# Kernel optimization log

Hardware: AMD Instinct MI355X
Metric: run time of the kernel (lower is better)

## Reference

```python
import jax, jax.numpy as jnp
import numpy as np

N_E = 1024
E_DIM = 64
BETA = 0.25


def setup_inputs() -> dict:
    key = jax.random.key(0)
    k_z, k_c = jax.random.split(key)
    z = jax.random.normal(k_z, (64, E_DIM, 32, 32), dtype=jnp.float32)  # [B, e_dim, H, W]
    # Codebook initialized uniform(-1/n_e, 1/n_e) as in the torch module
    codebook = jax.random.uniform(k_c, (N_E, E_DIM), dtype=jnp.float32,
                                  minval=-1.0 / N_E, maxval=1.0 / N_E)
    return {"z": z, "codebook": codebook}


def reference(z, codebook):
    beta = BETA
    n_e, e_dim = codebook.shape
    # [B, e_dim, H, W] -> [B, H, W, e_dim]
    z_nhwc = jnp.transpose(z, (0, 2, 3, 1))
    zf = z_nhwc.reshape(-1, e_dim)  # [N, e_dim]
    # Squared Euclidean distances: ||z||^2 + ||e||^2 - 2 z.e  -> [N, n_e]
    d = (jnp.sum(zf * zf, axis=1, keepdims=True)
         + jnp.sum(codebook * codebook, axis=1)
         - 2.0 * jnp.matmul(zf, codebook.T))
    min_encoding_indices = jnp.argmin(d, axis=1)[:, None]  # [N, 1]
    min_encodings = jax.nn.one_hot(min_encoding_indices[:, 0], n_e, dtype=zf.dtype)  # [N, n_e]
    # Gather codebook rows via one-hot matmul (same math as torch version)
    z_q = jnp.matmul(min_encodings, codebook).reshape(z_nhwc.shape)  # [B,H,W,e_dim]
    sg = jax.lax.stop_gradient
    loss = (jnp.mean((sg(z_nhwc) - z_q) ** 2)
            + beta * jnp.mean((z_nhwc - sg(z_q)) ** 2))
    # Straight-through estimator
    z_q = z_nhwc + sg(z_q - z_nhwc)
    z_q = jnp.transpose(z_q, (0, 3, 1, 2))  # back to [B, e_dim, H, W]
    return (loss, z_q, min_encodings, min_encoding_indices)
```

## Files before the change

kernel.cpp:

```cpp
#include <hip/hip_runtime.h>

#define N_ROWS 65536
#define NE 1024
#define ED 64
#define ERR_GAP 8e-5f

static const size_t OFF_ZQ = 1;
static const size_t OFF_ME = 1 + 4194304;
static const size_t OFF_IDX = OFF_ME + (size_t)N_ROWS * NE;
#define ME_FLOATS ((size_t)N_ROWS * NE)

#define SC_CBF  0
#define SC_Z2   65536
#define SC_FLAG 131072
#define SC_CAND 196608

typedef __attribute__((ext_vector_type(8))) short short8v;
typedef __attribute__((ext_vector_type(4))) float f32x4;

__device__ __forceinline__ unsigned bf16_rne(float v) {
  unsigned u = __float_as_uint(v);
  return (u + 0x7FFFu + ((u >> 16) & 1u)) >> 16;
}

__device__ __forceinline__ void gld16(const void* g, void* l) {
  __builtin_amdgcn_global_load_lds(
      (const __attribute__((address_space(1))) void*)g,
      (__attribute__((address_space(3))) void*)l, 16, 0, 0);
}

__global__ __launch_bounds__(256) void k_fill(float* __restrict__ me) {
  const size_t n4 = (ME_FLOATS - 3) >> 2;
  float4* __restrict__ p4 = reinterpret_cast<float4*>(me + 3);
  const size_t stride = (size_t)gridDim.x * blockDim.x;
  const float4 zero4 = make_float4(0.f, 0.f, 0.f, 0.f);
  for (size_t i = blockIdx.x * (size_t)blockDim.x + threadIdx.x; i < n4; i += stride)
    p4[i] = zero4;
  if (blockIdx.x == 0 && threadIdx.x == 0) {
    me[0] = 0.f; me[1] = 0.f; me[2] = 0.f;
    me[ME_FLOATS - 1] = 0.f;
  }
}

__global__ __launch_bounds__(256) void k_e2cb(const float* __restrict__ cb,
                                              float* __restrict__ e2,
                                              short* __restrict__ cbfrag) {
  const int tid = blockIdx.x * 256 + threadIdx.x;
  const int ct = tid >> 6, lane = tid & 63;
  const int col = ct * 16 + (lane & 15);
  const int k0 = (lane >> 4) * 8;
  const float* __restrict__ ep = cb + (size_t)col * ED + k0;
  short* __restrict__ o = cbfrag + (size_t)ct * 2048 + lane * 8;
  #pragma unroll
  for (int ks = 0; ks < 2; ++ks) {
    short h[8], lo[8];
    #pragma unroll
    for (int i = 0; i < 8; ++i) {
      const float v = ep[ks * 32 + i];
      const unsigned hb = bf16_rne(v);
      const float res = v - __uint_as_float(hb << 16);
      h[i] = (short)hb; lo[i] = (short)bf16_rne(res);
    }
    *(short8v*)(o + (size_t)(0 * 2 + ks) * 512) = *(short8v*)h;
    *(short8v*)(o + (size_t)(1 * 2 + ks) * 512) = *(short8v*)lo;
  }
  if (threadIdx.x < 64) {
    const int j = blockIdx.x * 64 + threadIdx.x;
    const float* __restrict__ e = cb + (size_t)j * ED;
    float r[8];
    #pragma unroll
    for (int i = 0; i < 8; ++i) {
      float v = e[i]; float q = v * v;
      asm volatile("" : "+v"(q)); r[i] = q;
    }
    #pragma unroll
    for (int k = 1; k < 8; ++k)
      #pragma unroll
      for (int i = 0; i < 8; ++i) {
        float v = e[8 * k + i]; float q = v * v;
        asm volatile("" : "+v"(q)); r[i] += q;
      }
    e2[j] = ((r[0] + r[1]) + (r[2] + r[3])) + ((r[4] + r[5]) + (r[6] + r[7]));
  }
}

__global__ __launch_bounds__(256, 4) void k_dist(const float* __restrict__ z,
    const short* __restrict__ cbfrag, const float* __restrict__ e2g,
    float* __restrict__ z2g, float* __restrict__ idxf, int* __restrict__ flag,
    int* __restrict__ cand) {
  __shared__ float4 smem4[2320];
  short* lBs = (short*)smem4;
  float* e2l = (float*)(smem4 + 2048);
  float* z2l = (float*)(smem4 + 2304);
  float (*lzf)[65] = (float(*)[65])smem4;

  const int t = threadIdx.x, w = t >> 6, lane = t & 63;
  const int row0 = blockIdx.x * 64;

  gld16(e2g + w * 256 + lane * 4, e2l + w * 256);

  const int rl = w * 16 + (lane & 15);
  const int n0 = row0 + rl;
  const int bb = n0 >> 10, hw = n0 & 1023;
  const float* __restrict__ zp = z + (size_t)bb * 65536 + hw;
  const int k0 = (lane >> 4) * 8;
  #pragma unroll
  for (int ks = 0; ks < 2; ++ks)
    #pragma unroll
    for (int i = 0; i < 8; ++i)
      lzf[ks * 32 + k0 + i][rl] = zp[(size_t)(ks * 32 + k0 + i) << 10];
  __syncthreads();

  short8v a[2][2];
  #pragma unroll
  for (int ks = 0; ks < 2; ++ks) {
    short h[8], lo[8];
    #pragma unroll
    for (int i = 0; i < 8; ++i) {
      const float v = lzf[ks * 32 + k0 + i][rl];
      const unsigned hb = bf16_rne(v);
      const float res = v - __uint_as_float(hb << 16);
      h[i] = (short)hb; lo[i] = (short)bf16_rne(res);
    }
    a[0][ks] = *(short8v*)h;
    a[1][ks] = *(short8v*)lo;
  }
  if (t < 64) {
    float r[8];
    #pragma unroll
    for (int i = 0; i < 8; ++i) {
      const float v = lzf[i][t];
      float q = v * v; asm volatile("" : "+v"(q)); r[i] = q;
    }
    #pragma unroll
    for (int k = 1; k < 8; ++k)
      #pragma unroll
      for (int i = 0; i < 8; ++i) {
        const float v = lzf[8 * k + i][t];
        float q = v * v; asm volatile("" : "+v"(q)); r[i] += q;
      }
    const float z2v = ((r[0] + r[1]) + (r[2] + r[3])) + ((r[4] + r[5]) + (r[6] + r[7]));
    z2g[row0 + t] = z2v;
    z2l[t] = z2v;
  }
  __syncthreads();

  #pragma unroll
  for (int i = 0; i < 4; ++i) {
    const int s = w * 4 + i;
    gld16(cbfrag + s * 512 + lane * 8, lBs + s * 512);
  }
  float z2r[4];
  #pragma unroll
  for (int reg = 0; reg < 4; ++reg)
    z2r[reg] = z2l[w * 16 + (lane >> 4) * 4 + reg];
  float Tm1[4], Tm2[4], Tm3[4]; int Tb1[4], Tb2[4];
  #pragma unroll
  for (int reg = 0; reg < 4; ++reg) {
    Tm1[reg] = 1e30f; Tm2[reg] = 1e30f; Tm3[reg] = 1e30f;
    Tb1[reg] = 0; Tb2[reg] = 0;
  }
  __syncthreads();

  int buf = 0;
  for (int c = 0; c < 16; ++c) {
    if (c < 15) {
      #pragma unroll
      for (int i = 0; i < 4; ++i) {
        const int s = w * 4 + i;
        gld16(cbfrag + (size_t)(c + 1) * 8192 + s * 512 + lane * 8,
              lBs + (buf ^ 1) * 8192 + s * 512);
      }
    }
    #pragma unroll 1
    for (int ctl = 0; ctl < 4; ++ctl) {
      short8v bfr[2][2];
      #pragma unroll
      for (int hl = 0; hl < 2; ++hl)
        #pragma unroll
        for (int ks = 0; ks < 2; ++ks)
          bfr[hl][ks] = *(const short8v*)(lBs + buf * 8192 +
              (ctl * 4 + hl * 2 + ks) * 512 + lane * 8);

      f32x4 acc = (f32x4)(0.0f);
      #pragma unroll
      for (int p = 0; p < 3; ++p) {
        const int pa = (p == 2) ? 1 : 0;
        const int pb = (p == 1) ? 1 : 0;
        #pragma unroll
        for (int ks = 0; ks < 2; ++ks)
          acc = __builtin_amdgcn_mfma_f32_16x16x32_bf16(a[pa][ks], bfr[pb][ks], acc, 0, 0, 0);
      }
      const int j = c * 64 + ctl * 16 + (lane & 15);
      const float e2v = e2l[j];
      #pragma unroll
      for (int reg = 0; reg < 4; ++reg) {
        const float dd = (z2r[reg] + e2v) - 2.0f * acc[reg];
        if (dd < Tm1[reg]) {
          Tm3[reg] = Tm2[reg]; Tm2[reg] = Tm1[reg]; Tb2[reg] = Tb1[reg];
          Tm1[reg] = dd; Tb1[reg] = j;
        } else if (dd < Tm2[reg]) {
          Tm3[reg] = Tm2[reg]; Tm2[reg] = dd; Tb2[reg] = j;
        } else if (dd < Tm3[reg]) {
          Tm3[reg] = dd;
        }
      }
    }
    __syncthreads();
    buf ^= 1;
  }

  #pragma unroll
  for (int reg = 0; reg < 4; ++reg) {
    float rm = Tm1[reg]; int ri = Tb1[reg];
    #pragma unroll
    for (int off = 1; off < 16; off <<= 1) {
      const float om = __shfl_xor(rm, off, 64);
      const int   oi = __shfl_xor(ri, off, 64);
      if (om < rm || (om == rm && oi < ri)) { rm = om; ri = oi; }
    }
    const float thr = rm + ERR_GAP;
    const bool c1 = (Tm1[reg] <= thr);
    const bool c2 = (Tm2[reg] <= thr);
    const bool c3 = (Tm3[reg] <= thr);
    const unsigned long long b1 = __ballot(c1);
    const unsigned long long b2 = __ballot(c2);
    const unsigned long long b3 = __ballot(c3);
    const int grp = lane >> 4;
    const unsigned m1m = (unsigned)((b1 >> (grp * 16)) & 0xFFFFull);
    const unsigned m2m = (unsigned)((b2 >> (grp * 16)) & 0xFFFFull);
    const unsigned m3m = (unsigned)((b3 >> (grp * 16)) & 0xFFFFull);
    const int n1 = __popc(m1m);
    const int ncand = n1 + __popc(m2m);
    const bool ovf = (m3m != 0u) || (ncand > 8);
    const int n = row0 + w * 16 + grp * 4 + reg;
    if (!ovf) {
      const unsigned below = (1u << (lane & 15)) - 1u;
      if (c1) cand[n * 8 + __popc(m1m & below)] = Tb1[reg];
      if (c2) cand[n * 8 + n1 + __popc(m2m & below)] = Tb2[reg];
    }
    if ((lane & 15) == 0) {
      idxf[n] = (float)ri;
      flag[n] = ovf ? 999 : (ncand >= 2 ? ncand : 0);
    }
  }
}

__global__ __launch_bounds__(256) void k_exactC(const float* __restrict__ z,
    const float* __restrict__ cb, const float* __restrict__ e2g,
    const float* __restrict__ z2g, const int* __restrict__ flag,
    const int* __restrict__ cand, float* __restrict__ idxf) {
  const int w = threadIdx.x >> 6, lane = threadIdx.x & 63;
  const int g = blockIdx.x * 4 + w;
  const int f = flag[g * 64 + lane];
  unsigned long long mask = __ballot(f != 0);
  while (mask) {
    const int bit = __ffsll((long long)mask) - 1; mask &= mask - 1;
    const int n = g * 64 + bit;
    const int fn = __shfl(f, bit, 64);
    const int b = n >> 10, hw = n & 1023;
    const float zv = z[(size_t)b * 65536 + ((size_t)lane << 10) + hw];
    const float z2v = z2g[n];
    if (fn != 999) {
      const int ci = cand[n * 8 + (lane < fn ? lane : 0)];
      const float* __restrict__ e = cb + (size_t)ci * ED;
      float acl = 0.f;
      #pragma unroll
      for (int k = 0; k < ED; ++k)
        acl = fmaf(__shfl(zv, k, 64), e[k], acl);
      float d = (z2v + e2g[ci]) - 2.0f * acl;
      int bi = ci;
      if (lane >= fn) { d = 1e30f; bi = 0x7FFFFFFF; }
      #pragma unroll
      for (int off = 1; off < 8; off <<= 1) {
        const float om = __shfl_xor(d, off, 64);
        const int   oi = __shfl_xor(bi, off, 64);
        if (om < d || (om == d && oi < bi)) { d = om; bi = oi; }
      }
      if (lane == 0) idxf[n] = (float)bi;
    } else {
      float bm = 1e30f; int bi = 0;
      #pragma unroll 1
      for (int q = 0; q < 16; ++q) {
        const int j = lane * 16 + q;
        const float4* __restrict__ e4 = (const float4*)(cb + (size_t)j * ED);
        float acl = 0.f;
        #pragma unroll
        for (int p = 0; p < 16; ++p) {
          const float4 ee = e4[p];
          acl = fmaf(__shfl(zv, 4 * p + 0, 64), ee.x, acl);
          acl = fmaf(__shfl(zv, 4 * p + 1, 64), ee.y, acl);
          acl = fmaf(__shfl(zv, 4 * p + 2, 64), ee.z, acl);
          acl = fmaf(__shfl(zv, 4 * p + 3, 64), ee.w, acl);
        }
        const float d = (z2v + e2g[j]) - 2.0f * acl;
        if (d < bm) { bm = d; bi = j; }
      }
      #pragma unroll
      for (int off = 1; off < 64; off <<= 1) {
        const float om = __shfl_xor(bm, off, 64);
        const int   oi = __shfl_xor(bi, off, 64);
        if (om < bm || (om == bm && oi < bi)) { bm = om; bi = oi; }
      }
      if (lane == 0) idxf[n] = (float)bi;
    }
  }
}

__global__ __launch_bounds__(256) void k_zq(const float* __restrict__ z,
    const float* __restrict__ cb, const float* __restrict__ idxf,
    float* __restrict__ zq, float* __restrict__ partial, float* __restrict__ me) {
  float s = 0.f;
  #pragma unroll 1
  for (int it = 0; it < 8; ++it) {
    const int o = (it * 2048 + blockIdx.x) * 256 + threadIdx.x;
    const int b = o >> 16;
    const int d = (o >> 10) & 63;
    const int hw = o & 1023;
    const int n = (b << 10) + hw;
    const int idx = (int)idxf[n];
    const float v = cb[(size_t)idx * ED + d];
    zq[o] = v;
    if (d == 0) me[(size_t)n * NE + idx] = 1.0f;
    const float diff = z[o] - v;
    s = fmaf(diff, diff, s);
  }
  #pragma unroll
  for (int off = 32; off > 0; off >>= 1) s += __shfl_xor(s, off, 64);
  __shared__ float sh[4];
  if ((threadIdx.x & 63) == 0) sh[threadIdx.x >> 6] = s;
  __syncthreads();
  if (threadIdx.x == 0)
    partial[blockIdx.x] = (sh[0] + sh[1]) + (sh[2] + sh[3]);
}

__global__ void k_loss(const float* __restrict__ partial, float* __restrict__ out0) {
  const int t = threadIdx.x;
  double s = 0.0;
  #pragma unroll
  for (int k = 0; k < 8; ++k) s += (double)partial[t + (k << 8)];
  #pragma unroll
  for (int off = 32; off > 0; off >>= 1) s += __shfl_xor(s, off, 64);
  __shared__ double sh[4];
  if ((t & 63) == 0) sh[t >> 6] = s;
  __syncthreads();
  if (t == 0)
    out0[0] = (float)(1.25 * ((sh[0] + sh[1]) + (sh[2] + sh[3])) / 4194304.0);
}

extern "C" void kernel_launch(void* const* d_in, const int* in_sizes, int n_in,
                              void* d_out, int out_size, void* d_ws, size_t ws_size,
                              hipStream_t stream) {
  const float* z  = (const float*)d_in[0];
  const float* cb = (const float*)d_in[1];
  float* out  = (float*)d_out;
  float* zq   = out + OFF_ZQ;
  float* me   = out + OFF_ME;
  float* idxf = out + OFF_IDX;
  float* sbase = out + 4;
  short* cbfrag = (short*)(sbase + SC_CBF);
  float* z2     = sbase + SC_Z2;
  int*   flag   = (int*)(sbase + SC_FLAG);
  int*   cand   = (int*)(sbase + SC_CAND);
  float* e2      = (float*)((char*)d_ws + 16);
  float* partial = (float*)((char*)d_ws + 4112);

  k_fill<<<2048, 256, 0, stream>>>(me);
  k_e2cb<<<16, 256, 0, stream>>>(cb, e2, cbfrag);
  k_dist<<<1024, 256, 0, stream>>>(z, cbfrag, e2, z2, idxf, flag, cand);
  k_exactC<<<256, 256, 0, stream>>>(z, cb, e2, z2, flag, cand, idxf);
  k_zq<<<2048, 256, 0, stream>>>(z, cb, idxf, zq, partial, me);
  k_loss<<<1, 256, 0, stream>>>(partial, out);
}
```

Measured before the change: 197.2 us.

## Fuse exact candidate refinement into distance kernel and write one-hot in one pass

Folds the candidate re-check (previously a separate k_exactC launch) into the distance kernel, keeping candidates, flags, z-norms and codebook norms in shared memory instead of global scratch. Replaces the separate zero-fill of the 256 MB one-hot matrix plus scattered 1.0 writes with a single kernel that writes every one-hot element directly, and folds the loss reduction into that kernel's block 0. This removes one full write pass over the one-hot output and two launches. In exchange, the distance blocks now do the serial refinement loop themselves, which may lengthen that kernel for rows that need a full scan.

```diff
diff --git a/kernel.cpp b/kernel.cpp
--- a/kernel.cpp
+++ b/kernel.cpp
@@ -11,9 +11,6 @@
 #define ME_FLOATS ((size_t)N_ROWS * NE)
 
 #define SC_CBF  0
-#define SC_Z2   65536
-#define SC_FLAG 131072
-#define SC_CAND 196608
 
 typedef __attribute__((ext_vector_type(8))) short short8v;
 typedef __attribute__((ext_vector_type(4))) float f32x4;
@@ -27,19 +24,6 @@
   __builtin_amdgcn_global_load_lds(
       (const __attribute__((address_space(1))) void*)g,
       (__attribute__((address_space(3))) void*)l, 16, 0, 0);
-}
-
-__global__ __launch_bounds__(256) void k_fill(float* __restrict__ me) {
-  const size_t n4 = (ME_FLOATS - 3) >> 2;
-  float4* __restrict__ p4 = reinterpret_cast<float4*>(me + 3);
-  const size_t stride = (size_t)gridDim.x * blockDim.x;
-  const float4 zero4 = make_float4(0.f, 0.f, 0.f, 0.f);
-  for (size_t i = blockIdx.x * (size_t)blockDim.x + threadIdx.x; i < n4; i += stride)
-    p4[i] = zero4;
-  if (blockIdx.x == 0 && threadIdx.x == 0) {
-    me[0] = 0.f; me[1] = 0.f; me[2] = 0.f;
-    me[ME_FLOATS - 1] = 0.f;
-  }
 }
 
 __global__ __launch_bounds__(256) void k_e2cb(const float* __restrict__ cb,
@@ -84,15 +68,16 @@
   }
 }
 
-__global__ __launch_bounds__(256, 4) void k_dist(const float* __restrict__ z,
-    const short* __restrict__ cbfrag, const float* __restrict__ e2g,
-    float* __restrict__ z2g, float* __restrict__ idxf, int* __restrict__ flag,
-    int* __restrict__ cand) {
+__global__ __launch_bounds__(256, 4) void k_distX(const float* __restrict__ z,
+    const float* __restrict__ cb, const short* __restrict__ cbfrag,
+    const float* __restrict__ e2g, float* __restrict__ idxf) {
   __shared__ float4 smem4[2320];
   short* lBs = (short*)smem4;
   float* e2l = (float*)(smem4 + 2048);
   float* z2l = (float*)(smem4 + 2304);
   float (*lzf)[65] = (float(*)[65])smem4;
+  int* candL = (int*)smem4;
+  int* nfl   = (int*)smem4 + 512;
 
   const int t = threadIdx.x, w = t >> 6, lane = t & 63;
   const int row0 = blockIdx.x * 64;
@@ -139,9 +124,7 @@
         const float v = lzf[8 * k + i][t];
         float q = v * v; asm volatile("" : "+v"(q)); r[i] += q;
       }
-    const float z2v = ((r[0] + r[1]) + (r[2] + r[3])) + ((r[4] + r[5]) + (r[6] + r[7]));
-    z2g[row0 + t] = z2v;
-    z2l[t] = z2v;
+    z2l[t] = ((r[0] + r[1]) + (r[2] + r[3])) + ((r[4] + r[5]) + (r[6] + r[7]));
   }
   __syncthreads();
 
@@ -233,42 +216,37 @@
     const int n1 = __popc(m1m);
     const int ncand = n1 + __popc(m2m);
     const bool ovf = (m3m != 0u) || (ncand > 8);
-    const int n = row0 + w * 16 + grp * 4 + reg;
+    const int rowLocal = w * 16 + grp * 4 + reg;
     if (!ovf) {
       const unsigned below = (1u << (lane & 15)) - 1u;
-      if (c1) cand[n * 8 + __popc(m1m & below)] = Tb1[reg];
-      if (c2) cand[n * 8 + n1 + __popc(m2m & below)] = Tb2[reg];
+      if (c1) candL[rowLocal * 8 + __popc(m1m & below)] = Tb1[reg];
+      if (c2) candL[rowLocal * 8 + n1 + __popc(m2m & below)] = Tb2[reg];
     }
     if ((lane & 15) == 0) {
-      idxf[n] = (float)ri;
-      flag[n] = ovf ? 999 : (ncand >= 2 ? ncand : 0);
-    }
-  }
-}
-
-__global__ __launch_bounds__(256) void k_exactC(const float* __restrict__ z,
-    const float* __restrict__ cb, const float* __restrict__ e2g,
-    const float* __restrict__ z2g, const int* __restrict__ flag,
-    const int* __restrict__ cand, float* __restrict__ idxf) {
-  const int w = threadIdx.x >> 6, lane = threadIdx.x & 63;
-  const int g = blockIdx.x * 4 + w;
-  const int f = flag[g * 64 + lane];
-  unsigned long long mask = __ballot(f != 0);
-  while (mask) {
-    const int bit = __ffsll((long long)mask) - 1; mask &= mask - 1;
-    const int n = g * 64 + bit;
-    const int fn = __shfl(f, bit, 64);
-    const int b = n >> 10, hw = n & 1023;
-    const float zv = z[(size_t)b * 65536 + ((size_t)lane << 10) + hw];
-    const float z2v = z2g[n];
+      const bool wrf = ovf || (ncand >= 2);
+      nfl[rowLocal] = ovf ? 999 : (ncand >= 2 ? ncand : 0);
+      if (!wrf) idxf[row0 + rowLocal] = (float)ri;
+    }
+  }
+  __syncthreads();
+
+  #pragma unroll 1
+  for (int r = 0; r < 16; ++r) {
+    const int rowLocal = w * 16 + r;
+    const int fn = nfl[rowLocal];
+    if (fn == 0) continue;
+    const int n = row0 + rowLocal;
+    const int b2 = n >> 10, hw2 = n & 1023;
+    const float zv = z[(size_t)b2 * 65536 + ((size_t)lane << 10) + hw2];
+    const float z2v = z2l[rowLocal];
     if (fn != 999) {
-      const int ci = cand[n * 8 + (lane < fn ? lane : 0)];
+      const int ci = candL[rowLocal * 8 + (lane < fn ? lane : 0)];
       const float* __restrict__ e = cb + (size_t)ci * ED;
       float acl = 0.f;
-      #pragma unroll
+      #pragma unroll 8
       for (int k = 0; k < ED; ++k)
         acl = fmaf(__shfl(zv, k, 64), e[k], acl);
-      float d = (z2v + e2g[ci]) - 2.0f * acl;
+      float d = (z2v + e2l[ci]) - 2.0f * acl;
       int bi = ci;
       if (lane >= fn) { d = 1e30f; bi = 0x7FFFFFFF; }
       #pragma unroll
@@ -293,7 +271,7 @@
           acl = fmaf(__shfl(zv, 4 * p + 2, 64), ee.z, acl);
           acl = fmaf(__shfl(zv, 4 * p + 3, 64), ee.w, acl);
         }
-        const float d = (z2v + e2g[j]) - 2.0f * acl;
+        const float d = (z2v + e2l[j]) - 2.0f * acl;
         if (d < bm) { bm = d; bi = j; }
       }
       #pragma unroll
@@ -309,7 +287,7 @@
 
 __global__ __launch_bounds__(256) void k_zq(const float* __restrict__ z,
     const float* __restrict__ cb, const float* __restrict__ idxf,
-    float* __restrict__ zq, float* __restrict__ partial, float* __restrict__ me) {
+    float* __restrict__ zq, float* __restrict__ partial) {
   float s = 0.f;
   #pragma unroll 1
   for (int it = 0; it < 8; ++it) {
@@ -321,7 +299,6 @@
     const int idx = (int)idxf[n];
     const float v = cb[(size_t)idx * ED + d];
     zq[o] = v;
-    if (d == 0) me[(size_t)n * NE + idx] = 1.0f;
     const float diff = z[o] - v;
     s = fmaf(diff, diff, s);
   }
@@ -334,18 +311,54 @@
     partial[blockIdx.x] = (sh[0] + sh[1]) + (sh[2] + sh[3]);
 }
 
-__global__ void k_loss(const float* __restrict__ partial, float* __restrict__ out0) {
+__global__ __launch_bounds__(256) void k_onehot(const float* __restrict__ idxf,
+    const float* __restrict__ partial, float* __restrict__ me,
+    float* __restrict__ out0) {
+  __shared__ int idxL[32];
   const int t = threadIdx.x;
-  double s = 0.0;
-  #pragma unroll
-  for (int k = 0; k < 8; ++k) s += (double)partial[t + (k << 8)];
-  #pragma unroll
-  for (int off = 32; off > 0; off >>= 1) s += __shfl_xor(s, off, 64);
-  __shared__ double sh[4];
-  if ((t & 63) == 0) sh[t >> 6] = s;
-  __syncthreads();
-  if (t == 0)
-    out0[0] = (float)(1.25 * ((sh[0] + sh[1]) + (sh[2] + sh[3])) / 4194304.0);
+  const int n0 = blockIdx.x * 32;
+  if (t < 32) idxL[t] = (int)idxf[n0 + t];
+  __syncthreads();
+  float* __restrict__ base = me + (size_t)n0 * 1024;
+  float4* __restrict__ p4 = (float4*)(base + 3);
+  #pragma unroll 1
+  for (int s = t; s < 8191; s += 256) {
+    const int f0 = 3 + 4 * s;
+    const int row = f0 >> 10;
+    const int col0 = f0 & 1023;
+    float4 v;
+    if (col0 <= 1020) {
+      const int idx = idxL[row];
+      v.x = (col0 == idx)     ? 1.0f : 0.0f;
+      v.y = (col0 + 1 == idx) ? 1.0f : 0.0f;
+      v.z = (col0 + 2 == idx) ? 1.0f : 0.0f;
+      v.w = (col0 + 3 == idx) ? 1.0f : 0.0f;
+    } else {
+      v.x = (idxL[row] == 1023)    ? 1.0f : 0.0f;
+      v.y = (idxL[row + 1] == 0)   ? 1.0f : 0.0f;
+      v.z = (idxL[row + 1] == 1)   ? 1.0f : 0.0f;
+      v.w = (idxL[row + 1] == 2)   ? 1.0f : 0.0f;
+    }
+    p4[s] = v;
+  }
+  if (t == 0) {
+    base[0] = (idxL[0] == 0) ? 1.0f : 0.0f;
+    base[1] = (idxL[0] == 1) ? 1.0f : 0.0f;
+    base[2] = (idxL[0] == 2) ? 1.0f : 0.0f;
+    base[32767] = (idxL[31] == 1023) ? 1.0f : 0.0f;
+  }
+  if (blockIdx.x == 0) {
+    double sd = 0.0;
+    #pragma unroll
+    for (int k = 0; k < 8; ++k) sd += (double)partial[t + (k << 8)];
+    #pragma unroll
+    for (int off = 32; off > 0; off >>= 1) sd += __shfl_xor(sd, off, 64);
+    __shared__ double shd[4];
+    if ((t & 63) == 0) shd[t >> 6] = sd;
+    __syncthreads();
+    if (t == 0)
+      out0[0] = (float)(1.25 * ((shd[0] + shd[1]) + (shd[2] + shd[3])) / 4194304.0);
+  }
 }
 
 extern "C" void kernel_launch(void* const* d_in, const int* in_sizes, int n_in,
@@ -359,16 +372,11 @@
   float* idxf = out + OFF_IDX;
   float* sbase = out + 4;
   short* cbfrag = (short*)(sbase + SC_CBF);
-  float* z2     = sbase + SC_Z2;
-  int*   flag   = (int*)(sbase + SC_FLAG);
-  int*   cand   = (int*)(sbase + SC_CAND);
   float* e2      = (float*)((char*)d_ws + 16);
   float* partial = (float*)((char*)d_ws + 4112);
 
-  k_fill<<<2048, 256, 0, stream>>>(me);
   k_e2cb<<<16, 256, 0, stream>>>(cb, e2, cbfrag);
-  k_dist<<<1024, 256, 0, stream>>>(z, cbfrag, e2, z2, idxf, flag, cand);
-  k_exactC<<<256, 256, 0, stream>>>(z, cb, e2, z2, flag, cand, idxf);
-  k_zq<<<2048, 256, 0, stream>>>(z, cb, idxf, zq, partial, me);
-  k_loss<<<1, 256, 0, stream>>>(partial, out);
-}
+  k_distX<<<1024, 256, 0, stream>>>(z, cb, cbfrag, e2, idxf);
+  k_zq<<<2048, 256, 0, stream>>>(z, cb, idxf, zq, partial);
+  k_onehot<<<2048, 256, 0, stream>>>(idxf, partial, me, out);
+}
```

After: 164.4 us, median of 3. -16.6%, faster.
